# Performance work log

Hardware: AMD Instinct MI355X
Metric: run time of the kernel (lower is better)

The kernel has to match this reference:

```python
import jax, jax.numpy as jnp
import numpy as np

B, I, C, L, KS = 16, 64, 128, 16384, 5
CA_K = 5
K_CR = 76      # crucial channels: floor(0.6*128)=76, already even
EPS = 1e-5


def conv1d(x, w, pad):
    # x: [N, Cin, L], w: [Cout, Cin, K]
    return jax.lax.conv_general_dilated(
        x, w, window_strides=(1,), padding=[(pad, pad)],
        dimension_numbers=('NCH', 'OIH', 'NCH'))


def bn(x, g, b, m, v):
    # eval-mode BatchNorm1d over channel dim of [N, C, L]
    inv = g / jnp.sqrt(v + EPS)
    return x * inv[None, :, None] + (b - m * inv)[None, :, None]


def setup_inputs() -> dict:
    key = jax.random.key(0)
    ks = jax.random.split(key, 10)
    return {
        'x': jax.random.normal(ks[0], (B, I, L), jnp.float32),
        'conv_w': jax.random.normal(ks[1], (C, I, KS), jnp.float32) / np.sqrt(I * KS).astype(np.float32),
        'conv_b': jax.random.normal(ks[2], (C,), jnp.float32) * 0.01,
        'bn_g': jnp.ones((C,), jnp.float32) + jax.random.normal(ks[3], (C,), jnp.float32) * 0.05,
        'bn_b': jax.random.normal(ks[4], (C,), jnp.float32) * 0.05,
        'bn_m': jax.random.normal(ks[5], (C,), jnp.float32) * 0.05,
        'bn_v': jnp.ones((C,), jnp.float32) + jax.random.uniform(ks[6], (C,), jnp.float32) * 0.1,
        'alpha': jnp.float32(0.5),
        'beta': jnp.float32(0.5),
        'ca_w': jax.random.normal(ks[7], (1, 1, CA_K), jnp.float32) / np.sqrt(CA_K).astype(np.float32),
        'ca_b': jnp.zeros((1,), jnp.float32),
        'sa_w': jax.random.normal(ks[8], (1, 2, 7), jnp.float32) / np.sqrt(14.0).astype(np.float32),
        'sabn_g': jnp.ones((1,), jnp.float32) + jax.random.normal(ks[9], (1,), jnp.float32) * 0.05,
        'sabn_b': jnp.zeros((1,), jnp.float32),
        'sabn_m': jnp.zeros((1,), jnp.float32),
        'sabn_v': jnp.ones((1,), jnp.float32),
    }


def reference(x, conv_w, conv_b, bn_g, bn_b, bn_m, bn_v, alpha, beta,
              ca_w, ca_b, sa_w, sabn_g, sabn_b, sabn_m, sabn_v):
    # ---- conv_layer: Conv1d + BN + ReLU ----
    f = conv1d(x, conv_w, KS // 2) + conv_b[None, :, None]      # [B,C,L]
    f = jax.nn.relu(bn(f, bn_g, bn_b, bn_m, bn_v))

    # ---- ChannelAttention ----
    F_avg = jnp.mean(f, axis=2, keepdims=True)                  # [B,C,1]
    F_max = jnp.max(f, axis=2, keepdims=True)                   # [B,C,1]
    F_add = alpha * F_avg + 0.5 * (F_avg + F_max) + beta * F_max
    z = conv1d(F_add.transpose(0, 2, 1), ca_w, CA_K // 2) + ca_b[None, :, None]  # [B,1,C]
    channel_map = jax.nn.sigmoid(z.transpose(0, 2, 1))          # [B,C,1]

    crf = f * channel_map                                       # channel refined features

    # ---- SpatialAttention: topk channel split + scatter masks ----
    cm = channel_map[:, :, 0]                                   # [B,C]
    _, idx = jax.lax.top_k(cm, K_CR)                            # [B,K_CR]
    cru = jnp.zeros_like(cm).at[jnp.arange(B)[:, None], idx].set(1.0)[:, :, None]  # [B,C,1]
    sub = 1.0 - cru

    cf = cru * crf                                              # crucial features [B,C,L]
    sf = sub * crf                                              # subcrucial features

    c_max = jnp.max(cf, axis=1, keepdims=True)                  # [B,1,L]
    c_avg = jnp.mean(cf, axis=1, keepdims=True) * (C / K_CR)
    s_max = jnp.max(sf, axis=1, keepdims=True)
    s_avg = jnp.mean(sf, axis=1, keepdims=True) * (C / (C - K_CR))

    def gate(mx, av):
        y = conv1d(jnp.concatenate([mx, av], axis=1), sa_w, 3)  # [B,1,L]
        return jax.nn.sigmoid(jax.nn.relu(bn(y, sabn_g, sabn_b, sabn_m, sabn_v)))

    A1 = gate(c_max, c_avg)
    A2 = gate(s_max, s_avg)
    return cf * A1 + sf * A2                                    # [B,C,L]
```

## Files before the change

### kernel.cpp

```cpp
#include <hip/hip_runtime.h>
#include <hip/hip_bf16.h>
#include <math.h>

#define BB 16
#define IC 64
#define CH 128
#define LL 16384
#define KS 5
#define CAK 5
#define KCR 76
#define EPSV 1e-5f
#define NLT2 256

typedef short bf16x8 __attribute__((ext_vector_type(8)));
typedef float f32x16 __attribute__((ext_vector_type(16)));

#define OFF_WPACK 0
#define OFF_BIAS2 40960
#define OFF_PSUM  (OFF_BIAS2 + CH)
#define OFF_PMAX  (OFF_PSUM + BB*CH*NLT2)
#define OFF_CM    (OFF_PMAX + BB*CH*NLT2)
#define OFF_MASK  (OFF_CM + BB*CH)
#define OFF_A1    (OFF_MASK + BB*CH)
#define OFF_A2    (OFF_A1 + BB*LL)

__device__ __forceinline__ unsigned short f2bf(float f) {
    union { float f; unsigned u; } v; v.f = f;
    return (unsigned short)((v.u + 0x7FFFu + ((v.u >> 16) & 1u)) >> 16);
}
__device__ __forceinline__ float bf2f(unsigned short h) {
    union { unsigned u; float f; } v; v.u = ((unsigned)h) << 16;
    return v.f;
}

template<int CTRL>
__device__ __forceinline__ float dppf(float v) {
    return __builtin_bit_cast(float,
        __builtin_amdgcn_update_dpp(0, __builtin_bit_cast(int, v), CTRL, 0xF, 0xF, true));
}
__device__ __forceinline__ float dpp_sum32(float s) {
    s += dppf<0x111>(s);
    s += dppf<0x112>(s);
    s += dppf<0x114>(s);
    s += dppf<0x118>(s);
    s += dppf<0x142>(s);
    return s;
}
__device__ __forceinline__ float dpp_max32(float m) {
    m = fmaxf(m, dppf<0x111>(m));
    m = fmaxf(m, dppf<0x112>(m));
    m = fmaxf(m, dppf<0x114>(m));
    m = fmaxf(m, dppf<0x118>(m));
    m = fmaxf(m, dppf<0x142>(m));
    return m;
}

__global__ void prep_kernel(const float* __restrict__ conv_w, const float* __restrict__ conv_b,
                            const float* __restrict__ bn_g, const float* __restrict__ bn_b,
                            const float* __restrict__ bn_m, const float* __restrict__ bn_v,
                            unsigned short* __restrict__ wpack, float* __restrict__ bias2)
{
    int e = blockIdx.x * 256 + threadIdx.x;
    if (e < 8 * 20 * 64 * 8) {
        int j    = e & 7;
        int ln   = (e >> 3) & 63;
        int rest = e >> 9;
        int s    = rest % 20;
        int mt   = (rest / 20) & 1;
        int ch2  = (rest / 40) & 1;
        int ver  = rest / 80;
        int c  = ch2 * 64 + mt * 32 + (ln & 31);
        int kk = s >> 2;
        int i  = (s & 3) * 16 + (ln >> 5) * 8 + j;
        float inv = bn_g[c] * rsqrtf(bn_v[c] + EPSV);
        float w = conv_w[(c * IC + i) * KS + kk] * inv;
        unsigned short h = f2bf(w);
        wpack[e] = (ver == 0) ? h : f2bf(w - bf2f(h));
    }
    if (e < CH) {
        float inv = bn_g[e] * rsqrtf(bn_v[e] + EPSV);
        bias2[e] = (conv_b[e] - bn_m[e]) * inv + bn_b[e];
    }
}

__global__ __launch_bounds__(256, 4)
void conv_mfma_kernel(const float* __restrict__ x,
                      const unsigned short* __restrict__ wpack,
                      const float* __restrict__ bias2,
                      float* __restrict__ f,
                      float* __restrict__ psum, float* __restrict__ pmax)
{
    __shared__ unsigned short xs[136 * 128];
    const int b   = blockIdx.x;
    const int lt  = blockIdx.y;
    const int l0  = lt * 128;
    const int tid = threadIdx.x;
    const int ln  = tid & 63;
    const int wv  = __builtin_amdgcn_readfirstlane(tid >> 6);

    const float* xb = x + (size_t)b * (IC * LL);
    const int ibase = wv * 16;
    #pragma unroll
    for (int g = 0; g < 3; ++g) {
        int row = g * 64 + ln;
        int l   = l0 - 4 + row;
        if (row < 136) {
            bool vl = (l >= 0) && (l < LL);
            float v[16];
            #pragma unroll
            for (int q = 0; q < 16; ++q)
                v[q] = vl ? xb[(size_t)(ibase + q) * LL + l] : 0.0f;
            int rs = row & 7;
            #pragma unroll
            for (int q2 = 0; q2 < 4; ++q2) {
                unsigned short h[4], lo[4];
                #pragma unroll
                for (int j = 0; j < 4; ++j) {
                    float vv = v[q2 * 4 + j];
                    h[j]  = f2bf(vv);
                    lo[j] = f2bf(vv - bf2f(h[j]));
                }
                int i0   = ibase + q2 * 4;
                int cc   = (i0 >> 3) ^ rs;
                int epos = row * 128 + cc * 8 + (i0 & 7);
                uint2 wh, wl;
                wh.x = (unsigned)h[0]  | ((unsigned)h[1]  << 16);
                wh.y = (unsigned)h[2]  | ((unsigned)h[3]  << 16);
                wl.x = (unsigned)lo[0] | ((unsigned)lo[1] << 16);
                wl.y = (unsigned)lo[2] | ((unsigned)lo[3] << 16);
                *(uint2*)&xs[epos]      = wh;
                *(uint2*)&xs[epos + 64] = wl;
            }
        }
    }
    __syncthreads();

    const int ch2  = wv >> 1;
    const int lh   = wv & 1;
    const int ln31 = ln & 31;
    const int hi   = ln >> 5;
    const int rowbase = lh * 64 + ln31 + 2;

    const unsigned short* wp  = wpack + (size_t)ln * 8;
    const unsigned short* pA0 = wp + (size_t)((ch2 * 2 + 0) * 20) * 512;
    const unsigned short* pA1 = wp + (size_t)((ch2 * 2 + 1) * 20) * 512;
    const unsigned short* pA2 = wp + (size_t)(((2 + ch2) * 2 + 0) * 20) * 512;
    const unsigned short* pA3 = wp + (size_t)(((2 + ch2) * 2 + 1) * 20) * 512;

    f32x16 acc[2][2];
    #pragma unroll
    for (int mt = 0; mt < 2; ++mt)
        #pragma unroll
        for (int nt = 0; nt < 2; ++nt)
            #pragma unroll
            for (int r = 0; r < 16; ++r) acc[mt][nt][r] = 0.0f;

    auto loadA = [&](bf16x8* Av, int s) {
        Av[0] = *(const bf16x8*)(pA0 + (size_t)s * 512);
        Av[1] = *(const bf16x8*)(pA1 + (size_t)s * 512);
        Av[2] = *(const bf16x8*)(pA2 + (size_t)s * 512);
        Av[3] = *(const bf16x8*)(pA3 + (size_t)s * 512);
    };
    auto loadB = [&](bf16x8* Bv, int s) {
        int kk = s >> 2, iq = s & 3;
        int r0 = rowbase + kk;
        int r1 = r0 + 32;
        int c0 = ((iq << 1) + hi) ^ (r0 & 7);
        int c1 = ((iq << 1) + hi) ^ (r1 & 7);
        Bv[0] = *(const bf16x8*)&xs[r0 * 128 + c0 * 8];
        Bv[1] = *(const bf16x8*)&xs[r0 * 128 + 64 + c0 * 8];
        Bv[2] = *(const bf16x8*)&xs[r1 * 128 + c1 * 8];
        Bv[3] = *(const bf16x8*)&xs[r1 * 128 + 64 + c1 * 8];
    };
    auto compute = [&](const bf16x8* Av, const bf16x8* Bv) {
        acc[0][0] = __builtin_amdgcn_mfma_f32_32x32x16_bf16(Av[0], Bv[0], acc[0][0], 0, 0, 0);
        acc[1][0] = __builtin_amdgcn_mfma_f32_32x32x16_bf16(Av[1], Bv[0], acc[1][0], 0, 0, 0);
        acc[0][1] = __builtin_amdgcn_mfma_f32_32x32x16_bf16(Av[0], Bv[2], acc[0][1], 0, 0, 0);
        acc[1][1] = __builtin_amdgcn_mfma_f32_32x32x16_bf16(Av[1], Bv[2], acc[1][1], 0, 0, 0);
        acc[0][0] = __builtin_amdgcn_mfma_f32_32x32x16_bf16(Av[0], Bv[1], acc[0][0], 0, 0, 0);
        acc[1][0] = __builtin_amdgcn_mfma_f32_32x32x16_bf16(Av[1], Bv[1], acc[1][0], 0, 0, 0);
        acc[0][1] = __builtin_amdgcn_mfma_f32_32x32x16_bf16(Av[0], Bv[3], acc[0][1], 0, 0, 0);
        acc[1][1] = __builtin_amdgcn_mfma_f32_32x32x16_bf16(Av[1], Bv[3], acc[1][1], 0, 0, 0);
        acc[0][0] = __builtin_amdgcn_mfma_f32_32x32x16_bf16(Av[2], Bv[0], acc[0][0], 0, 0, 0);
        acc[1][0] = __builtin_amdgcn_mfma_f32_32x32x16_bf16(Av[3], Bv[0], acc[1][0], 0, 0, 0);
        acc[0][1] = __builtin_amdgcn_mfma_f32_32x32x16_bf16(Av[2], Bv[2], acc[0][1], 0, 0, 0);
        acc[1][1] = __builtin_amdgcn_mfma_f32_32x32x16_bf16(Av[3], Bv[2], acc[1][1], 0, 0, 0);
    };

    bf16x8 Ar[3][4], Br[2][4];
    loadA(Ar[0], 0); loadA(Ar[1], 1); loadA(Ar[2], 2);
    loadB(Br[0], 0); loadB(Br[1], 1);
    #pragma unroll
    for (int s = 0; s < 20; ++s) {
        compute(Ar[s % 3], Br[s & 1]);
        if (s + 3 < 20) loadA(Ar[s % 3], s + 3);
        if (s + 2 < 20) loadB(Br[s & 1], s + 2);
    }

    const int lgbase = l0 + lh * 64 + ln31;
    #pragma unroll
    for (int mt = 0; mt < 2; ++mt) {
        #pragma unroll
        for (int nt = 0; nt < 2; ++nt) {
            #pragma unroll
            for (int r = 0; r < 16; ++r) {
                int c = ch2 * 64 + mt * 32 + (r & 3) + 8 * (r >> 2) + 4 * hi;
                float fv = fmaxf(acc[mt][nt][r] + bias2[c], 0.0f);
                f[((size_t)(b * CH + c)) * LL + lgbase + nt * 32] = fv;
                acc[mt][nt][r] = fv;
            }
        }
    }
    #pragma unroll
    for (int mt = 0; mt < 2; ++mt) {
        #pragma unroll
        for (int r = 0; r < 16; ++r) {
            float s = dpp_sum32(acc[mt][0][r] + acc[mt][1][r]);
            float m = dpp_max32(fmaxf(acc[mt][0][r], acc[mt][1][r]));
            if (ln31 == 31) {
                int c   = ch2 * 64 + mt * 32 + (r & 3) + 8 * (r >> 2) + 4 * hi;
                int lt2 = lt * 2 + lh;
                psum[(b * CH + c) * NLT2 + lt2] = s;
                pmax[(b * CH + c) * NLT2 + lt2] = m;
            }
        }
    }
}

__global__ void chan_kernel(const float* __restrict__ psum, const float* __restrict__ pmax,
                            const float* __restrict__ alpha, const float* __restrict__ beta,
                            const float* __restrict__ ca_w, const float* __restrict__ ca_b,
                            float* __restrict__ cm, float* __restrict__ maskv)
{
    int b = blockIdx.x;
    int c = threadIdx.x;
    const float* ps = psum + (b * CH + c) * NLT2;
    const float* pm = pmax + (b * CH + c) * NLT2;
    float s = 0.0f, m = 0.0f;
    for (int t = 0; t < NLT2; ++t) { s += ps[t]; m = fmaxf(m, pm[t]); }
    float favg = s * (1.0f / LL);
    float fadd = (alpha[0] + 0.5f) * favg + (beta[0] + 0.5f) * m;

    __shared__ float fa[CH];
    __shared__ float cms[CH];
    fa[c] = fadd;
    __syncthreads();

    float z = ca_b[0];
    #pragma unroll
    for (int k = 0; k < CAK; ++k) {
        int cc = c + k - 2;
        float v = (cc >= 0 && cc < CH) ? fa[cc] : 0.0f;
        z = fmaf(ca_w[k], v, z);
    }
    float cmv = 1.0f / (1.0f + expf(-z));
    cms[c] = cmv;
    __syncthreads();

    int rank = 0;
    for (int cc = 0; cc < CH; ++cc) {
        float o = cms[cc];
        rank += (o > cmv || (o == cmv && cc < c)) ? 1 : 0;
    }
    cm[b * CH + c] = cmv;
    maskv[b * CH + c] = (rank < KCR) ? 1.0f : 0.0f;
}

__global__ __launch_bounds__(256)
void stats_gate_kernel(const float* __restrict__ f, const float* __restrict__ cm,
                       const float* __restrict__ maskv, const float* __restrict__ sa_w,
                       const float* __restrict__ sabn_g, const float* __restrict__ sabn_b,
                       const float* __restrict__ sabn_m, const float* __restrict__ sabn_v,
                       float* __restrict__ A1, float* __restrict__ A2)
{
    __shared__ float cms[CH], mks[CH];
    __shared__ float st[4][264];
    int b   = blockIdx.x;
    int l0  = blockIdx.y * 256;
    int tid = threadIdx.x;
    if (tid < CH) { cms[tid] = cm[b * CH + tid]; mks[tid] = maskv[b * CH + tid]; }
    __syncthreads();

    for (int idx = tid; idx < 262; idx += 256) {
        int l = l0 - 3 + idx;
        float cmx = 0.f, csm = 0.f, smx = 0.f, ssm = 0.f;
        if (l >= 0 && l < LL) {
            const float* fb = f + (size_t)b * CH * LL + l;
            #pragma unroll 4
            for (int c = 0; c < CH; ++c) {
                float v  = fb[(size_t)c * LL] * cms[c];
                float mk = mks[c];
                float vs = v * mk;
                float vu = v - vs;
                cmx = fmaxf(cmx, vs);
                smx = fmaxf(smx, vu);
                csm += vs;
                ssm += vu;
            }
        }
        st[0][idx] = cmx;
        st[1][idx] = csm * (1.0f / KCR);
        st[2][idx] = smx;
        st[3][idx] = ssm * (1.0f / (CH - KCR));
    }
    __syncthreads();

    float inv = sabn_g[0] * rsqrtf(sabn_v[0] + EPSV);
    float bb2 = sabn_b[0] - sabn_m[0] * inv;
    float y1 = 0.f, y2 = 0.f;
    #pragma unroll
    for (int k = 0; k < 7; ++k) {
        float wm = sa_w[k], wa = sa_w[7 + k];
        y1 = fmaf(wm, st[0][tid + k], fmaf(wa, st[1][tid + k], y1));
        y2 = fmaf(wm, st[2][tid + k], fmaf(wa, st[3][tid + k], y2));
    }
    float t1 = fmaxf(y1 * inv + bb2, 0.f);
    float t2 = fmaxf(y2 * inv + bb2, 0.f);
    A1[b * LL + l0 + tid] = 1.0f / (1.0f + expf(-t1));
    A2[b * LL + l0 + tid] = 1.0f / (1.0f + expf(-t2));
}

__global__ __launch_bounds__(256)
void final_kernel(float* __restrict__ out, const float* __restrict__ cm,
                  const float* __restrict__ maskv,
                  const float* __restrict__ A1, const float* __restrict__ A2)
{
    int g = blockIdx.x * 256 + threadIdx.x;
    size_t idx4 = (size_t)g * 4;
    int l  = (int)(idx4 & (LL - 1));
    int bc = (int)(idx4 >> 14);
    int b  = bc >> 7;
    float cmv = cm[bc];
    float mk  = maskv[bc];
    const float* Ap = (mk > 0.5f) ? A1 : A2;
    float4 a = *(const float4*)&Ap[b * LL + l];
    float4 v = *(const float4*)&out[idx4];
    v.x *= cmv * a.x;
    v.y *= cmv * a.y;
    v.z *= cmv * a.z;
    v.w *= cmv * a.w;
    *(float4*)&out[idx4] = v;
}

extern "C" void kernel_launch(void* const* d_in, const int* in_sizes, int n_in,
                              void* d_out, int out_size, void* d_ws, size_t ws_size,
                              hipStream_t stream)
{
    const float* x      = (const float*)d_in[0];
    const float* conv_w = (const float*)d_in[1];
    const float* conv_b = (const float*)d_in[2];
    const float* bn_g   = (const float*)d_in[3];
    const float* bn_b   = (const float*)d_in[4];
    const float* bn_m   = (const float*)d_in[5];
    const float* bn_v   = (const float*)d_in[6];
    const float* alpha  = (const float*)d_in[7];
    const float* beta   = (const float*)d_in[8];
    const float* ca_w   = (const float*)d_in[9];
    const float* ca_b   = (const float*)d_in[10];
    const float* sa_w   = (const float*)d_in[11];
    const float* sabn_g = (const float*)d_in[12];
    const float* sabn_b = (const float*)d_in[13];
    const float* sabn_m = (const float*)d_in[14];
    const float* sabn_v = (const float*)d_in[15];

    float* out = (float*)d_out;
    float* ws  = (float*)d_ws;

    unsigned short* wpack = (unsigned short*)(ws + OFF_WPACK);
    float* bias2 = ws + OFF_BIAS2;
    float* psum  = ws + OFF_PSUM;
    float* pmax  = ws + OFF_PMAX;
    float* cmv_  = ws + OFF_CM;
    float* mskv  = ws + OFF_MASK;
    float* A1p   = ws + OFF_A1;
    float* A2p   = ws + OFF_A2;

    prep_kernel<<<320, 256, 0, stream>>>(conv_w, conv_b, bn_g, bn_b, bn_m, bn_v, wpack, bias2);

    conv_mfma_kernel<<<dim3(BB, 128), 256, 0, stream>>>(x, wpack, bias2, out, psum, pmax);

    chan_kernel<<<BB, CH, 0, stream>>>(psum, pmax, alpha, beta, ca_w, ca_b, cmv_, mskv);

    stats_gate_kernel<<<dim3(BB, 64), 256, 0, stream>>>(out, cmv_, mskv, sa_w,
                                                        sabn_g, sabn_b, sabn_m, sabn_v, A1p, A2p);

    final_kernel<<<(BB * CH * LL / 4 + 255) / 256, 256, 0, stream>>>(out, cmv_, mskv, A1p, A2p);
}
```

Before: 177.5 us.

## Store conv output as fp16 intermediate and fuse spatial stats with final scaling

The conv kernel now writes its ReLU output as fp16 into a workspace buffer, so the intermediate tensor traffic is halved. A new fused kernel computes the spatial max/avg statistics, the 7-tap gate conv and sigmoid, and then writes the final output in one pass. This removes the separate A1/A2 buffers and the final kernel's re-read of the fp32 tensor. It adds fp16 rounding error on the intermediate features and only runs when the workspace is large enough; otherwise the old path is used.

After: 168.0 us. 5.4% less time.

```diff
diff --git a/kernel.cpp b/kernel.cpp
--- a/kernel.cpp
+++ b/kernel.cpp
@@ -23,6 +23,8 @@
 #define OFF_MASK  (OFF_CM + BB*CH)
 #define OFF_A1    (OFF_MASK + BB*CH)
 #define OFF_A2    (OFF_A1 + BB*LL)
+#define OFF_F16   (OFF_A2 + BB*LL)
+#define WS_NEED_FLOATS ((size_t)OFF_F16 + (size_t)BB * CH * LL / 2)
 
 __device__ __forceinline__ unsigned short f2bf(float f) {
     union { float f; unsigned u; } v; v.f = f;
@@ -31,6 +33,14 @@
 __device__ __forceinline__ float bf2f(unsigned short h) {
     union { unsigned u; float f; } v; v.u = ((unsigned)h) << 16;
     return v.f;
+}
+__device__ __forceinline__ unsigned short f2h(float f) {
+    _Float16 h = (_Float16)f;
+    return __builtin_bit_cast(unsigned short, h);
+}
+__device__ __forceinline__ float h2f(unsigned short u) {
+    _Float16 h = __builtin_bit_cast(_Float16, u);
+    return (float)h;
 }
 
 template<int CTRL>
@@ -83,11 +93,12 @@
     }
 }
 
+template<bool F16OUT>
 __global__ __launch_bounds__(256, 4)
 void conv_mfma_kernel(const float* __restrict__ x,
                       const unsigned short* __restrict__ wpack,
                       const float* __restrict__ bias2,
-                      float* __restrict__ f,
+                      void* __restrict__ fout,
                       float* __restrict__ psum, float* __restrict__ pmax)
 {
     __shared__ unsigned short xs[136 * 128];
@@ -206,7 +217,9 @@
             for (int r = 0; r < 16; ++r) {
                 int c = ch2 * 64 + mt * 32 + (r & 3) + 8 * (r >> 2) + 4 * hi;
                 float fv = fmaxf(acc[mt][nt][r] + bias2[c], 0.0f);
-                f[((size_t)(b * CH + c)) * LL + lgbase + nt * 32] = fv;
+                size_t off = ((size_t)(b * CH + c)) * LL + lgbase + nt * 32;
+                if constexpr (F16OUT) ((unsigned short*)fout)[off] = f2h(fv);
+                else                  ((float*)fout)[off] = fv;
                 acc[mt][nt][r] = fv;
             }
         }
@@ -264,6 +277,70 @@
     }
     cm[b * CH + c] = cmv;
     maskv[b * CH + c] = (rank < KCR) ? 1.0f : 0.0f;
+}
+
+__global__ __launch_bounds__(256)
+void sgf_kernel(const unsigned short* __restrict__ f16, float* __restrict__ out,
+                const float* __restrict__ cm, const float* __restrict__ maskv,
+                const float* __restrict__ sa_w,
+                const float* __restrict__ sabn_g, const float* __restrict__ sabn_b,
+                const float* __restrict__ sabn_m, const float* __restrict__ sabn_v)
+{
+    __shared__ float cms[CH], mks[CH];
+    __shared__ float st[4][264];
+    const int g   = blockIdx.x;
+    const int b   = blockIdx.y;
+    const int l0  = g * 256;
+    const int tid = threadIdx.x;
+    if (tid < CH) { cms[tid] = cm[b * CH + tid]; mks[tid] = maskv[b * CH + tid]; }
+    __syncthreads();
+
+    for (int idx = tid; idx < 262; idx += 256) {
+        int l = l0 - 3 + idx;
+        float cmx = 0.f, csm = 0.f, smx = 0.f, ssm = 0.f;
+        if (l >= 0 && l < LL) {
+            const unsigned short* fb = f16 + (size_t)b * CH * LL + l;
+            #pragma unroll 4
+            for (int c = 0; c < CH; ++c) {
+                float v  = h2f(fb[(size_t)c * LL]) * cms[c];
+                float mk = mks[c];
+                float vs = v * mk;
+                float vu = v - vs;
+                cmx = fmaxf(cmx, vs);
+                smx = fmaxf(smx, vu);
+                csm += vs;
+                ssm += vu;
+            }
+        }
+        st[0][idx] = cmx;
+        st[1][idx] = csm * (1.0f / KCR);
+        st[2][idx] = smx;
+        st[3][idx] = ssm * (1.0f / (CH - KCR));
+    }
+    __syncthreads();
+
+    float inv = sabn_g[0] * rsqrtf(sabn_v[0] + EPSV);
+    float bb2 = sabn_b[0] - sabn_m[0] * inv;
+    float y1 = 0.f, y2 = 0.f;
+    #pragma unroll
+    for (int k = 0; k < 7; ++k) {
+        float wm = sa_w[k], wa = sa_w[7 + k];
+        y1 = fmaf(wm, st[0][tid + k], fmaf(wa, st[1][tid + k], y1));
+        y2 = fmaf(wm, st[2][tid + k], fmaf(wa, st[3][tid + k], y2));
+    }
+    float t1 = fmaxf(y1 * inv + bb2, 0.f);
+    float t2 = fmaxf(y2 * inv + bb2, 0.f);
+    float A1 = 1.0f / (1.0f + expf(-t1));
+    float A2 = 1.0f / (1.0f + expf(-t2));
+
+    const unsigned short* fb = f16 + (size_t)b * CH * LL + l0 + tid;
+    float* ob = out + (size_t)b * CH * LL + l0 + tid;
+    #pragma unroll 4
+    for (int c = 0; c < CH; ++c) {
+        float v = h2f(fb[(size_t)c * LL]) * cms[c];
+        float a = (mks[c] > 0.5f) ? A1 : A2;
+        ob[(size_t)c * LL] = v * a;
+    }
 }
 
 __global__ __launch_bounds__(256)
@@ -374,15 +451,24 @@
     float* mskv  = ws + OFF_MASK;
     float* A1p   = ws + OFF_A1;
     float* A2p   = ws + OFF_A2;
+    unsigned short* f16p = (unsigned short*)(ws + OFF_F16);
+
+    const bool fp16_path = (ws_size >= WS_NEED_FLOATS * sizeof(float));
 
     prep_kernel<<<320, 256, 0, stream>>>(conv_w, conv_b, bn_g, bn_b, bn_m, bn_v, wpack, bias2);
 
-    conv_mfma_kernel<<<dim3(BB, 128), 256, 0, stream>>>(x, wpack, bias2, out, psum, pmax);
-
-    chan_kernel<<<BB, CH, 0, stream>>>(psum, pmax, alpha, beta, ca_w, ca_b, cmv_, mskv);
-
-    stats_gate_kernel<<<dim3(BB, 64), 256, 0, stream>>>(out, cmv_, mskv, sa_w,
-                                                        sabn_g, sabn_b, sabn_m, sabn_v, A1p, A2p);
-
-    final_kernel<<<(BB * CH * LL / 4 + 255) / 256, 256, 0, stream>>>(out, cmv_, mskv, A1p, A2p);
-}
+    if (fp16_path) {
+        conv_mfma_kernel<true><<<dim3(BB, 128), 256, 0, stream>>>(x, wpack, bias2,
+                                                                  (void*)f16p, psum, pmax);
+        chan_kernel<<<BB, CH, 0, stream>>>(psum, pmax, alpha, beta, ca_w, ca_b, cmv_, mskv);
+        sgf_kernel<<<dim3(64, BB), 256, 0, stream>>>(f16p, out, cmv_, mskv, sa_w,
+                                                     sabn_g, sabn_b, sabn_m, sabn_v);
+    } else {
+        conv_mfma_kernel<false><<<dim3(BB, 128), 256, 0, stream>>>(x, wpack, bias2,
+                                                                   (void*)out, psum, pmax);
+        chan_kernel<<<BB, CH, 0, stream>>>(psum, pmax, alpha, beta, ca_w, ca_b, cmv_, mskv);
+        stats_gate_kernel<<<dim3(BB, 64), 256, 0, stream>>>(out, cmv_, mskv, sa_w,
+                                                            sabn_g, sabn_b, sabn_m, sabn_v, A1p, A2p);
+        final_kernel<<<(BB * CH * LL / 4 + 255) / 256, 256, 0, stream>>>(out, cmv_, mskv, A1p, A2p);
+    }
+}
```
